# Performance work log

Measured on AMD Instinct MI355X. Metric: run time of the kernel, lower is better.

Reference implementation:

```python
import jax, jax.numpy as jnp
import numpy as np

B, DIN, H, DOUT = 8192, 1024, 2048, 1024
P, E = 4, 6            # n_patches, n_edges
C = H // P             # per-patch feature dim = 512
IDX_I = jnp.array([0, 0, 0, 1, 1, 2])  # i<j pair order matches nested loop
IDX_J = jnp.array([1, 2, 3, 2, 3, 3])


def setup_inputs() -> dict:
    key = jax.random.key(0)
    ks = jax.random.split(key, 12)
    s = 0.02
    return {
        "x": jax.random.normal(ks[0], (B, DIN), jnp.float32),
        "fiber": jax.random.normal(ks[1], (B, C), jnp.float32),  # randn_like(base) in torch fwd
        "W_in": jax.random.normal(ks[2], (DIN, H), jnp.float32) * s,
        "b_in": jnp.zeros((H,), jnp.float32),
        "incidence": jax.random.normal(ks[3], (E, P), jnp.float32) * 0.1,
        "sheaf_maps": jnp.tile((jnp.eye(C, dtype=jnp.float32) * 0.1)[None], (E, 1, 1)),
        "damping": jnp.float32(0.1),
        "Wb": jax.random.normal(ks[4], (P, C, C // 2), jnp.float32) * s,
        "bb": jnp.zeros((P, C // 2), jnp.float32),
        "Wf": jax.random.normal(ks[5], (P, C, C // 2), jnp.float32) * s,
        "bf": jnp.zeros((P, C // 2), jnp.float32),
        "Wt": jax.random.normal(ks[6], (C, C), jnp.float32) * s,
        "bt": jnp.zeros((C,), jnp.float32),
        "Wr": jax.random.normal(ks[7], (E, C, C // 2), jnp.float32) * s,
        "br": jnp.zeros((E, C // 2), jnp.float32),
        "Wg": jax.random.normal(ks[8], (H, H), jnp.float32) * s,
        "bg": jnp.zeros((H,), jnp.float32),
        "Wc": jax.random.normal(ks[9], (H + C, DOUT), jnp.float32) * s,
        "bc": jnp.zeros((DOUT,), jnp.float32),
    }


def reference(x, fiber, W_in, b_in, incidence, sheaf_maps, damping,
              Wb, bb, Wf, bf, Wt, bt, Wr, br, Wg, bg, Wc, bc):
    # input projection + split into P contiguous chunks (stack == reshape)
    h = x @ W_in + b_in                                      # [B, H]
    sections = h.reshape(B, P, C)                            # [B, P, C]

    # --- NeuralSheafLaplacian ---
    # coboundary: incidence-weighted combination of patch sections, then per-edge sheaf map
    weighted = jnp.einsum('ep,bpc->bec', incidence, sections)          # [B, E, C]
    coboundary = jnp.einsum('bec,ecd->bed', weighted, sheaf_maps)      # [B, E, C]
    L = incidence.T @ incidence                                        # [P, P] = delta^T delta
    diffused = sections - damping * jnp.einsum('pq,bqc->bpc', L, sections)
    h1_norm = jnp.linalg.norm(coboundary, axis=-1).mean(axis=-1)       # [B]

    # --- FiberBundleLayer ---
    base = diffused.mean(axis=1)                                       # [B, C]
    b_proj = jnp.einsum('bc,scd->bsd', base, Wb) + bb                  # [B, P, C/2]
    f_proj = jnp.einsum('bc,scd->bsd', fiber, Wf) + bf                 # [B, P, C/2]
    simplices = jnp.concatenate([b_proj, f_proj], axis=-1) @ Wt + bt   # [B, P, C]
    total = simplices.mean(axis=1)                                     # [B, C]

    # --- CohomologyConsistency ---
    si = diffused[:, IDX_I]                                            # [B, E, C]
    sj = diffused[:, IDX_J]                                            # [B, E, C]
    ri = jnp.einsum('bec,ecd->bed', si, Wr) + br
    rj = jnp.einsum('bec,ecd->bed', sj, Wr) + br
    h1_loss = jnp.mean((ri - rj) ** 2, axis=(0, 2)).mean()             # mean of per-pair MSEs
    glued = diffused.reshape(B, H) @ Wg + bg                           # cat(sections) == reshape

    output = jnp.concatenate([glued, total], axis=-1) @ Wc + bc        # [B, DOUT]
    return output, diffused, h1_norm, h1_loss, total
```

## Files before the change

kernel.cpp:

```cpp
#include <hip/hip_runtime.h>
#include <cstdint>

#define B_    8192
#define DIN_  1024
#define H_    2048
#define DOUT_ 1024
#define P4_   4
#define E6_   6
#define C_    512
#define C2_   256

typedef __bf16 bf16x8 __attribute__((ext_vector_type(8)));
typedef float  f32x4  __attribute__((ext_vector_type(4)));

__device__ __forceinline__ unsigned short f2bf_bits(float f) {
    unsigned u = __float_as_uint(f);
    unsigned r = (u + 0x7fffu + ((u >> 16) & 1u)) >> 16;
    return (unsigned short)r;
}
__device__ __forceinline__ float bf2f(unsigned short s) {
    return __uint_as_float(((unsigned)s) << 16);
}

__device__ __forceinline__ void async_load16(void* lds, const void* g) {
    __builtin_amdgcn_global_load_lds(
        (__attribute__((address_space(1))) void*)(uintptr_t)g,
        (__attribute__((address_space(3))) void*)(unsigned int)(uintptr_t)lds,
        16, 0, 0);
}


__global__ void convert_f32_bf16_k(const float* __restrict__ in,
                                   unsigned short* __restrict__ out, int n) {
    int i = (blockIdx.x * blockDim.x + threadIdx.x) * 4;
    if (i + 3 < n) {
        float4 v = *(const float4*)(in + i);
        ushort4 o;
        o.x = f2bf_bits(v.x); o.y = f2bf_bits(v.y);
        o.z = f2bf_bits(v.z); o.w = f2bf_bits(v.w);
        *(ushort4*)(out + i) = o;
    }
}

__global__ void transpose_to_bf16_k(const float* __restrict__ in,
                                    unsigned short* __restrict__ out,
                                    int R, int Cc, long inStrideZ, long outStrideZ) {
    __shared__ float t[32][33];
    in  += (long)blockIdx.z * inStrideZ;
    out += (long)blockIdx.z * outStrideZ;
    int x0 = blockIdx.x << 5, y0 = blockIdx.y << 5;
    int tx = threadIdx.x, ty = threadIdx.y;
#pragma unroll
    for (int j = 0; j < 32; j += 8)
        t[ty + j][tx] = in[(long)(y0 + ty + j) * Cc + x0 + tx];
    __syncthreads();
#pragma unroll
    for (int j = 0; j < 32; j += 8)
        out[(long)(x0 + ty + j) * R + y0 + tx] = f2bf_bits(t[tx][ty + j]);
}

__global__ void wbar_k(const float* __restrict__ W, unsigned short* __restrict__ outT) {
    int id = blockIdx.x * blockDim.x + threadIdx.x;
    int d = id >> 9, c = id & 511;
    float s = 0.f;
#pragma unroll
    for (int si = 0; si < 4; si++) s += W[si * (512 * 256) + c * 256 + d];
    outT[id] = f2bf_bits(0.25f * s);
}

__global__ void bbar_k(const float* __restrict__ b, float* __restrict__ out) {
    int d = threadIdx.x;
    out[d] = 0.25f * (b[d] + b[256 + d] + b[512 + d] + b[768 + d]);
}

__global__ void k2_diffuse_k(const unsigned short* __restrict__ hb,
                             const float* __restrict__ incidence,
                             const float* __restrict__ damping,
                             float* __restrict__ outDiff,
                             unsigned short* __restrict__ diffb,
                             unsigned short* __restrict__ baseb,
                             unsigned short* __restrict__ weightedb,
                             unsigned short* __restrict__ debuf) {
    __shared__ float M4[4][4];
    __shared__ float inc2[24];
    int tid = threadIdx.x;
    if (tid < 16) {
        int p = tid >> 2, q = tid & 3;
        float l = 0.f;
#pragma unroll
        for (int e = 0; e < 6; e++) l += incidence[e * 4 + p] * incidence[e * 4 + q];
        M4[p][q] = (p == q ? 1.f : 0.f) - damping[0] * l;
    }
    if (tid < 24) inc2[tid] = incidence[tid];
    __syncthreads();

    int b = blockIdx.x >> 1;
    int c = ((blockIdx.x & 1) << 8) + tid;
    long hoff = (long)b * H_ + c;
    float s0 = bf2f(hb[hoff]);
    float s1 = bf2f(hb[hoff + 512]);
    float s2 = bf2f(hb[hoff + 1024]);
    float s3 = bf2f(hb[hoff + 1536]);

    float d0 = M4[0][0]*s0 + M4[0][1]*s1 + M4[0][2]*s2 + M4[0][3]*s3;
    float d1 = M4[1][0]*s0 + M4[1][1]*s1 + M4[1][2]*s2 + M4[1][3]*s3;
    float d2 = M4[2][0]*s0 + M4[2][1]*s1 + M4[2][2]*s2 + M4[2][3]*s3;
    float d3 = M4[3][0]*s0 + M4[3][1]*s1 + M4[3][2]*s2 + M4[3][3]*s3;

    outDiff[hoff]        = d0;
    outDiff[hoff + 512]  = d1;
    outDiff[hoff + 1024] = d2;
    outDiff[hoff + 1536] = d3;
    diffb[hoff]        = f2bf_bits(d0);
    diffb[hoff + 512]  = f2bf_bits(d1);
    diffb[hoff + 1024] = f2bf_bits(d2);
    diffb[hoff + 1536] = f2bf_bits(d3);
    baseb[(long)b * C_ + c] = f2bf_bits(0.25f * (d0 + d1 + d2 + d3));

#pragma unroll
    for (int e = 0; e < 6; e++) {
        float w = inc2[e*4+0]*s0 + inc2[e*4+1]*s1 + inc2[e*4+2]*s2 + inc2[e*4+3]*s3;
        weightedb[(long)e * (B_ * (long)C_) + (long)b * C_ + c] = f2bf_bits(w);
    }
    float dI[6] = {d0, d0, d0, d1, d1, d2};
    float dJ[6] = {d1, d2, d3, d2, d3, d3};
#pragma unroll
    for (int e = 0; e < 6; e++)
        debuf[(long)e * (B_ * (long)C_) + (long)b * C_ + c] = f2bf_bits(dI[e] - dJ[e]);
}

template <int MODE>
__global__ __launch_bounds__(256, 2)
void gemm_bt_k(const unsigned short* __restrict__ A, long sAz, int lda,
               const unsigned short* __restrict__ Bt, long sBz, int K,
               const float* __restrict__ bias,
               unsigned short* __restrict__ Cb, int ldcb,
               float* __restrict__ Cf, int ldcf,
               float* __restrict__ red, long sRz) {
    __shared__ __align__(16) unsigned short smA[128 * 64];
    __shared__ __align__(16) unsigned short smB[128 * 64];
    const int tid = threadIdx.x;
    const int lane = tid & 63, w = tid >> 6;
    const int wm = w >> 1, wn = w & 1;
    const int m16 = lane & 15, quad = lane >> 4;
    const int m7 = m16 & 7;
    A  += (long)blockIdx.z * sAz;
    Bt += (long)blockIdx.z * sBz;
    const long rowA0 = (long)blockIdx.y * 128;
    const long rowB0 = (long)blockIdx.x * 128;

    f32x4 acc[4][4];
#pragma unroll
    for (int i = 0; i < 4; i++)
#pragma unroll
        for (int j = 0; j < 4; j++) acc[i][j] = f32x4{0.f, 0.f, 0.f, 0.f};

    for (int k0 = 0; k0 < K; k0 += 64) {
#pragma unroll
        for (int i = 0; i < 4; i++) {
            int chunk = i * 256 + tid;
            int row = chunk >> 3;
            int keS = ((chunk & 7) ^ (row & 7)) << 3;
            async_load16(&smA[chunk << 3], A  + (rowA0 + row) * (long)lda + k0 + keS);
            async_load16(&smB[chunk << 3], Bt + (rowB0 + row) * (long)K   + k0 + keS);
        }
        __syncthreads();
#pragma unroll
        for (int kk = 0; kk < 64; kk += 32) {
            const int pc = (((kk >> 3) + quad) ^ m7) << 3;
            bf16x8 af[4], bfv[4];
#pragma unroll
            for (int i = 0; i < 4; i++) {
                af[i]  = *(const bf16x8*)&smA[((wm << 6) + (i << 4) + m16) * 64 + pc];
                bfv[i] = *(const bf16x8*)&smB[((wn << 6) + (i << 4) + m16) * 64 + pc];
            }
#pragma unroll
            for (int i = 0; i < 4; i++)
#pragma unroll
                for (int j = 0; j < 4; j++)
                    acc[i][j] = __builtin_amdgcn_mfma_f32_16x16x32_bf16(af[i], bfv[j], acc[i][j], 0, 0, 0);
        }
        __syncthreads();
    }

    const long rowBase = rowA0 + (wm << 6);
    const long colBase = rowB0 + (wn << 6);

    if (MODE <= 2) {
#pragma unroll
        for (int j = 0; j < 4; j++) {
            long col = colBase + (j << 4) + m16;
            float bv = bias ? bias[col] : 0.f;
#pragma unroll
            for (int i = 0; i < 4; i++) {
                long row = rowBase + (i << 4) + (quad << 2);
#pragma unroll
                for (int r = 0; r < 4; r++) {
                    float v = acc[i][j][r] + bv;
                    if (MODE == 0 || MODE == 2) Cb[(row + r) * (long)ldcb + col] = f2bf_bits(v);
                    if (MODE == 1 || MODE == 2) Cf[(row + r) * (long)ldcf + col] = v;
                }
            }
        }
    } else if (MODE == 3) {
        float* rz = red + (long)blockIdx.z * sRz;
#pragma unroll
        for (int i = 0; i < 4; i++) {
            float v0 = 0.f, v1 = 0.f, v2 = 0.f, v3 = 0.f;
#pragma unroll
            for (int j = 0; j < 4; j++) {
                float a0 = acc[i][j][0], a1 = acc[i][j][1], a2 = acc[i][j][2], a3 = acc[i][j][3];
                v0 += a0 * a0; v1 += a1 * a1; v2 += a2 * a2; v3 += a3 * a3;
            }
#pragma unroll
            for (int m = 1; m <= 8; m <<= 1) {
                v0 += __shfl_xor(v0, m); v1 += __shfl_xor(v1, m);
                v2 += __shfl_xor(v2, m); v3 += __shfl_xor(v3, m);
            }
            if (m16 == 0) {
                long row = rowBase + (i << 4) + (quad << 2);
                atomicAdd(&rz[row + 0], v0);
                atomicAdd(&rz[row + 1], v1);
                atomicAdd(&rz[row + 2], v2);
                atomicAdd(&rz[row + 3], v3);
            }
        }
    } else {
        float s = 0.f;
#pragma unroll
        for (int i = 0; i < 4; i++)
#pragma unroll
            for (int j = 0; j < 4; j++)
#pragma unroll
                for (int r = 0; r < 4; r++) { float a = acc[i][j][r]; s += a * a; }
#pragma unroll
        for (int m = 1; m <= 32; m <<= 1) s += __shfl_xor(s, m);
        if (lane == 0) atomicAdd(red, s);
    }
}

__global__ void f1_h1norm_k(const float* __restrict__ hn, float* __restrict__ out) {
    int b = blockIdx.x * 256 + threadIdx.x;
    float s = 0.f;
#pragma unroll
    for (int e = 0; e < 6; e++) s += sqrtf(hn[e * B_ + b]);
    out[b] = s * (1.f / 6.f);
}

__global__ void f2_h1loss_k(const float* __restrict__ acc, float* __restrict__ out) {
    if (threadIdx.x == 0) out[0] = acc[0] * (1.f / (8192.f * 6.f * 256.f));
}

extern "C" void kernel_launch(void* const* d_in, const int* in_sizes, int n_in,
                              void* d_out, int out_size, void* d_ws, size_t ws_size,
                              hipStream_t stream) {
    const float* x     = (const float*)d_in[0];
    const float* fiber = (const float*)d_in[1];
    const float* W_in  = (const float*)d_in[2];
    const float* b_in  = (const float*)d_in[3];
    const float* incid = (const float*)d_in[4];
    const float* sheaf = (const float*)d_in[5];
    const float* damp  = (const float*)d_in[6];
    const float* Wb    = (const float*)d_in[7];
    const float* bb    = (const float*)d_in[8];
    const float* Wf    = (const float*)d_in[9];
    const float* bfv   = (const float*)d_in[10];
    const float* Wt    = (const float*)d_in[11];
    const float* bt    = (const float*)d_in[12];
    const float* Wr    = (const float*)d_in[13];
    const float* Wg    = (const float*)d_in[15];
    const float* bg    = (const float*)d_in[16];
    const float* Wc    = (const float*)d_in[17];
    const float* bc    = (const float*)d_in[18];

    float* out      = (float*)d_out;
    float* outDiff  = out + 8388608;
    float* outH1n   = out + 25165824;
    float* outH1l   = out + 25174016;
    float* outTotal = out + 25174017;

    char* ws = (char*)d_ws;
    size_t o = 0;
    auto alloc = [&](size_t bytes) { size_t r = o; o += (bytes + 255) & ~(size_t)255; return r; };

    size_t r0 = alloc(50331648);
    unsigned short* xb = (unsigned short*)(ws + r0);
    unsigned short* hb = (unsigned short*)(ws + r0 + 16777216);
    unsigned short* Ab = (unsigned short*)(ws + r0);
    unsigned short* diffb     = (unsigned short*)(ws + alloc(33554432));
    unsigned short* baseb     = (unsigned short*)(ws + alloc(8388608));
    unsigned short* weightedb = (unsigned short*)(ws + alloc(50331648));
    unsigned short* debuf     = (unsigned short*)(ws + alloc(50331648));
    unsigned short* fiberb    = (unsigned short*)(ws + alloc(8388608));
    unsigned short* cbar      = (unsigned short*)(ws + alloc(8388608));
    unsigned short* WinT   = (unsigned short*)(ws + alloc(4194304));
    unsigned short* WgT    = (unsigned short*)(ws + alloc(8388608));
    unsigned short* WcT    = (unsigned short*)(ws + alloc(5242880));
    unsigned short* WtT    = (unsigned short*)(ws + alloc(524288));
    unsigned short* WrT    = (unsigned short*)(ws + alloc(1572864));
    unsigned short* ShT    = (unsigned short*)(ws + alloc(3145728));
    unsigned short* WbBarT = (unsigned short*)(ws + alloc(262144));
    unsigned short* WfBarT = (unsigned short*)(ws + alloc(262144));
    float* bbarf  = (float*)(ws + alloc(1024));
    float* bfbarf = (float*)(ws + alloc(1024));
    float* hnacc  = (float*)(ws + alloc(6 * 8192 * 4 + 256));
    float* lossacc = hnacc + 6 * 8192;

    (void)hipMemsetAsync(hnacc, 0, 6 * 8192 * 4 + 256, stream);

    convert_f32_bf16_k<<<8192, 256, 0, stream>>>(x, xb, 8388608);
    convert_f32_bf16_k<<<4096, 256, 0, stream>>>(fiber, fiberb, 4194304);
    dim3 tb(32, 8);
    transpose_to_bf16_k<<<dim3(64, 32), tb, 0, stream>>>(W_in, WinT, 1024, 2048, 0, 0);
    transpose_to_bf16_k<<<dim3(64, 64), tb, 0, stream>>>(Wg, WgT, 2048, 2048, 0, 0);
    transpose_to_bf16_k<<<dim3(32, 80), tb, 0, stream>>>(Wc, WcT, 2560, 1024, 0, 0);
    transpose_to_bf16_k<<<dim3(16, 16), tb, 0, stream>>>(Wt, WtT, 512, 512, 0, 0);
    transpose_to_bf16_k<<<dim3(16, 16, 6), tb, 0, stream>>>(sheaf, ShT, 512, 512, 512 * 512, 512 * 512);
    transpose_to_bf16_k<<<dim3(8, 16, 6), tb, 0, stream>>>(Wr, WrT, 512, 256, 512 * 256, 512 * 256);
    wbar_k<<<512, 256, 0, stream>>>(Wb, WbBarT);
    wbar_k<<<512, 256, 0, stream>>>(Wf, WfBarT);
    bbar_k<<<1, 256, 0, stream>>>(bb, bbarf);
    bbar_k<<<1, 256, 0, stream>>>(bfv, bfbarf);

    gemm_bt_k<0><<<dim3(16, 64, 1), 256, 0, stream>>>(xb, 0, DIN_, WinT, 0, DIN_,
                                                      b_in, hb, H_, nullptr, 0, nullptr, 0);
    k2_diffuse_k<<<16384, 256, 0, stream>>>(hb, incid, damp, outDiff, diffb, baseb, weightedb, debuf);

    gemm_bt_k<0><<<dim3(16, 64, 1), 256, 0, stream>>>(diffb, 0, H_, WgT, 0, H_,
                                                      bg, Ab, 2560, nullptr, 0, nullptr, 0);
    gemm_bt_k<3><<<dim3(4, 64, 6), 256, 0, stream>>>(weightedb, (long)B_ * C_, C_, ShT, (long)C_ * C_, C_,
                                                     nullptr, nullptr, 0, nullptr, 0, hnacc, B_);
    gemm_bt_k<4><<<dim3(2, 64, 6), 256, 0, stream>>>(debuf, (long)B_ * C_, C_, WrT, (long)C2_ * C_, C_,
                                                     nullptr, nullptr, 0, nullptr, 0, lossacc, 0);
    gemm_bt_k<0><<<dim3(2, 64, 1), 256, 0, stream>>>(baseb, 0, C_, WbBarT, 0, C_,
                                                     bbarf, cbar, C_, nullptr, 0, nullptr, 0);
    gemm_bt_k<0><<<dim3(2, 64, 1), 256, 0, stream>>>(fiberb, 0, C_, WfBarT, 0, C_,
                                                     bfbarf, cbar + 256, C_, nullptr, 0, nullptr, 0);
    gemm_bt_k<2><<<dim3(4, 64, 1), 256, 0, stream>>>(cbar, 0, C_, WtT, 0, C_,
                                                     bt, Ab + 2048, 2560, outTotal, C_, nullptr, 0);
    gemm_bt_k<1><<<dim3(8, 64, 1), 256, 0, stream>>>(Ab, 0, 2560, WcT, 0, 2560,
                                                     bc, nullptr, 0, out, DOUT_, nullptr, 0);
    f1_h1norm_k<<<32, 256, 0, stream>>>(hnacc, outH1n);
    f2_h1loss_k<<<1, 64, 0, stream>>>(lossacc, outH1l);

    (void)in_sizes; (void)n_in; (void)out_size; (void)ws_size;
}
```

Baseline: 622.6 us.

## Fold Wg into Wc to drop the glued GEMM and remap tile order

Precomputes a combined weight Wg·Wc_top (plus a folded bias bg·Wc_top + bc) so the final GEMM reads diffused sections directly. This removes the B×2048×2048 glued GEMM, replacing it with a small 1024×2048×2048 weight-only GEMM. k2_diffuse now writes its bf16 output straight into the 2560-wide concatenated buffer. Separately, the GEMM kernel remaps block IDs in groups of eight for better cache locality. The folding changes rounding: the product weight is formed in bf16, which may shift numerics slightly.

```diff
diff --git a/kernel.cpp b/kernel.cpp
--- a/kernel.cpp
+++ b/kernel.cpp
@@ -71,6 +71,24 @@
 __global__ void bbar_k(const float* __restrict__ b, float* __restrict__ out) {
     int d = threadIdx.x;
     out[d] = 0.25f * (b[d] + b[256 + d] + b[512 + d] + b[768 + d]);
+}
+
+__global__ void copy_wc_tail_k(const unsigned short* __restrict__ src,
+                               unsigned short* __restrict__ dst) {
+    int id = blockIdx.x * 256 + threadIdx.x;
+    int n = id >> 7, c4 = (id & 127) << 2;
+    long off = (long)n * 2560 + 2048 + c4;
+    *(ushort4*)(dst + off) = *(const ushort4*)(src + off);
+}
+
+__global__ void bout_k(const float* __restrict__ bg, const float* __restrict__ Wc,
+                       const float* __restrict__ bc, float* __restrict__ bout) {
+    int n = blockIdx.x * 256 + threadIdx.x;
+    int j0 = blockIdx.y << 7;
+    float s = (blockIdx.y == 0) ? bc[n] : 0.f;
+#pragma unroll 4
+    for (int j = 0; j < 128; j++) s += bg[j0 + j] * Wc[(long)(j0 + j) * 1024 + n];
+    atomicAdd(&bout[n], s);
 }
 
 __global__ void k2_diffuse_k(const unsigned short* __restrict__ hb,
@@ -97,6 +115,7 @@
     int b = blockIdx.x >> 1;
     int c = ((blockIdx.x & 1) << 8) + tid;
     long hoff = (long)b * H_ + c;
+    long doff = (long)b * 2560 + c;
     float s0 = bf2f(hb[hoff]);
     float s1 = bf2f(hb[hoff + 512]);
     float s2 = bf2f(hb[hoff + 1024]);
@@ -111,10 +130,10 @@
     outDiff[hoff + 512]  = d1;
     outDiff[hoff + 1024] = d2;
     outDiff[hoff + 1536] = d3;
-    diffb[hoff]        = f2bf_bits(d0);
-    diffb[hoff + 512]  = f2bf_bits(d1);
-    diffb[hoff + 1024] = f2bf_bits(d2);
-    diffb[hoff + 1536] = f2bf_bits(d3);
+    diffb[doff]        = f2bf_bits(d0);
+    diffb[doff + 512]  = f2bf_bits(d1);
+    diffb[doff + 1024] = f2bf_bits(d2);
+    diffb[doff + 1536] = f2bf_bits(d3);
     baseb[(long)b * C_ + c] = f2bf_bits(0.25f * (d0 + d1 + d2 + d3));
 
 #pragma unroll
@@ -144,10 +163,17 @@
     const int wm = w >> 1, wn = w & 1;
     const int m16 = lane & 15, quad = lane >> 4;
     const int m7 = m16 & 7;
+
+    const int nwg = gridDim.x * gridDim.y;
+    const int bid = blockIdx.y * gridDim.x + blockIdx.x;
+    const int lid = (nwg & 7) ? bid : (((bid & 7) * (nwg >> 3)) + (bid >> 3));
+    const int bx = lid % gridDim.x;
+    const int by = lid / gridDim.x;
+
     A  += (long)blockIdx.z * sAz;
     Bt += (long)blockIdx.z * sBz;
-    const long rowA0 = (long)blockIdx.y * 128;
-    const long rowB0 = (long)blockIdx.x * 128;
+    const long rowA0 = (long)by * 128;
+    const long rowB0 = (long)bx * 128;
 
     f32x4 acc[4][4];
 #pragma unroll
@@ -286,16 +312,16 @@
     size_t r0 = alloc(50331648);
     unsigned short* xb = (unsigned short*)(ws + r0);
     unsigned short* hb = (unsigned short*)(ws + r0 + 16777216);
-    unsigned short* Ab = (unsigned short*)(ws + r0);
-    unsigned short* diffb     = (unsigned short*)(ws + alloc(33554432));
+    unsigned short* Ab2560    = (unsigned short*)(ws + alloc(41943040));
     unsigned short* baseb     = (unsigned short*)(ws + alloc(8388608));
     unsigned short* weightedb = (unsigned short*)(ws + alloc(50331648));
     unsigned short* debuf     = (unsigned short*)(ws + alloc(50331648));
     unsigned short* fiberb    = (unsigned short*)(ws + alloc(8388608));
     unsigned short* cbar      = (unsigned short*)(ws + alloc(8388608));
     unsigned short* WinT   = (unsigned short*)(ws + alloc(4194304));
-    unsigned short* WgT    = (unsigned short*)(ws + alloc(8388608));
+    unsigned short* Wgb    = (unsigned short*)(ws + alloc(8388608));
     unsigned short* WcT    = (unsigned short*)(ws + alloc(5242880));
+    unsigned short* WoutT  = (unsigned short*)(ws + alloc(5242880));
     unsigned short* WtT    = (unsigned short*)(ws + alloc(524288));
     unsigned short* WrT    = (unsigned short*)(ws + alloc(1572864));
     unsigned short* ShT    = (unsigned short*)(ws + alloc(3145728));
@@ -303,16 +329,18 @@
     unsigned short* WfBarT = (unsigned short*)(ws + alloc(262144));
     float* bbarf  = (float*)(ws + alloc(1024));
     float* bfbarf = (float*)(ws + alloc(1024));
+    float* boutf  = (float*)(ws + alloc(4096));
     float* hnacc  = (float*)(ws + alloc(6 * 8192 * 4 + 256));
     float* lossacc = hnacc + 6 * 8192;
 
     (void)hipMemsetAsync(hnacc, 0, 6 * 8192 * 4 + 256, stream);
+    (void)hipMemsetAsync(boutf, 0, 4096, stream);
 
     convert_f32_bf16_k<<<8192, 256, 0, stream>>>(x, xb, 8388608);
     convert_f32_bf16_k<<<4096, 256, 0, stream>>>(fiber, fiberb, 4194304);
+    convert_f32_bf16_k<<<4096, 256, 0, stream>>>(Wg, Wgb, 4194304);
     dim3 tb(32, 8);
     transpose_to_bf16_k<<<dim3(64, 32), tb, 0, stream>>>(W_in, WinT, 1024, 2048, 0, 0);
-    transpose_to_bf16_k<<<dim3(64, 64), tb, 0, stream>>>(Wg, WgT, 2048, 2048, 0, 0);
     transpose_to_bf16_k<<<dim3(32, 80), tb, 0, stream>>>(Wc, WcT, 2560, 1024, 0, 0);
     transpose_to_bf16_k<<<dim3(16, 16), tb, 0, stream>>>(Wt, WtT, 512, 512, 0, 0);
     transpose_to_bf16_k<<<dim3(16, 16, 6), tb, 0, stream>>>(sheaf, ShT, 512, 512, 512 * 512, 512 * 512);
@@ -322,12 +350,15 @@
     bbar_k<<<1, 256, 0, stream>>>(bb, bbarf);
     bbar_k<<<1, 256, 0, stream>>>(bfv, bfbarf);
 
+    gemm_bt_k<0><<<dim3(16, 8, 1), 256, 0, stream>>>(WcT, 0, 2560, Wgb, 0, H_,
+                                                     nullptr, WoutT, 2560, nullptr, 0, nullptr, 0);
+    copy_wc_tail_k<<<512, 256, 0, stream>>>(WcT, WoutT);
+    bout_k<<<dim3(4, 16), 256, 0, stream>>>(bg, Wc, bc, boutf);
+
     gemm_bt_k<0><<<dim3(16, 64, 1), 256, 0, stream>>>(xb, 0, DIN_, WinT, 0, DIN_,
                                                       b_in, hb, H_, nullptr, 0, nullptr, 0);
-    k2_diffuse_k<<<16384, 256, 0, stream>>>(hb, incid, damp, outDiff, diffb, baseb, weightedb, debuf);
-
-    gemm_bt_k<0><<<dim3(16, 64, 1), 256, 0, stream>>>(diffb, 0, H_, WgT, 0, H_,
-                                                      bg, Ab, 2560, nullptr, 0, nullptr, 0);
+    k2_diffuse_k<<<16384, 256, 0, stream>>>(hb, incid, damp, outDiff, Ab2560, baseb, weightedb, debuf);
+
     gemm_bt_k<3><<<dim3(4, 64, 6), 256, 0, stream>>>(weightedb, (long)B_ * C_, C_, ShT, (long)C_ * C_, C_,
                                                      nullptr, nullptr, 0, nullptr, 0, hnacc, B_);
     gemm_bt_k<4><<<dim3(2, 64, 6), 256, 0, stream>>>(debuf, (long)B_ * C_, C_, WrT, (long)C2_ * C_, C_,
@@ -337,9 +368,9 @@
     gemm_bt_k<0><<<dim3(2, 64, 1), 256, 0, stream>>>(fiberb, 0, C_, WfBarT, 0, C_,
                                                      bfbarf, cbar + 256, C_, nullptr, 0, nullptr, 0);
     gemm_bt_k<2><<<dim3(4, 64, 1), 256, 0, stream>>>(cbar, 0, C_, WtT, 0, C_,
-                                                     bt, Ab + 2048, 2560, outTotal, C_, nullptr, 0);
-    gemm_bt_k<1><<<dim3(8, 64, 1), 256, 0, stream>>>(Ab, 0, 2560, WcT, 0, 2560,
-                                                     bc, nullptr, 0, out, DOUT_, nullptr, 0);
+                                                     bt, Ab2560 + 2048, 2560, outTotal, C_, nullptr, 0);
+    gemm_bt_k<1><<<dim3(8, 64, 1), 256, 0, stream>>>(Ab2560, 0, 2560, WoutT, 0, 2560,
+                                                     boutf, nullptr, 0, out, DOUT_, nullptr, 0);
     f1_h1norm_k<<<32, 256, 0, stream>>>(hnacc, outH1n);
     f2_h1loss_k<<<1, 64, 0, stream>>>(lossacc, outH1l);
 
```

New measurement: 586.0 us. 5.9% less time.
